# Optimization experiments

Measured on AMD Instinct MI355X. Metric: run time of the kernel, lower is better.

The kernel has to match this reference:

```python
import jax, jax.numpy as jnp
import numpy as np

N_NODES = 100000
N_EDGES = 3200000
IN_CH = 256
OUT_CH = 128


def setup_inputs() -> dict:
    key = jax.random.key(0)
    k1, k2, k3, k4, k5 = jax.random.split(key, 5)
    x = jax.random.normal(k1, (N_NODES, IN_CH), dtype=jnp.float32)
    edge_src = jax.random.randint(k2, (N_EDGES,), 0, N_NODES, dtype=jnp.int64 if jax.config.jax_enable_x64 else jnp.int32)
    edge_dst = jax.random.randint(k3, (N_EDGES,), 0, N_NODES, dtype=jnp.int64 if jax.config.jax_enable_x64 else jnp.int32)
    edge_vals = jax.random.uniform(k4, (N_EDGES,), dtype=jnp.float32)
    weight = jax.random.normal(k5, (IN_CH, OUT_CH), dtype=jnp.float32) * (2.0 / (IN_CH + OUT_CH)) ** 0.5  # glorot
    bias = jnp.zeros((OUT_CH,), dtype=jnp.float32)
    return {"x": x, "edge_src": edge_src, "edge_dst": edge_dst,
            "edge_vals": edge_vals, "weight": weight, "bias": bias}


def reference(x, edge_src, edge_dst, edge_vals, weight, bias):
    # out = A @ (x @ W) + b, with A given in COO form (edge_src=row, edge_dst=col, edge_vals)
    xw = x @ weight                                  # [N, out]
    msgs = xw[edge_dst] * edge_vals[:, None]         # gather source features, scale by edge weight
    agg = jax.ops.segment_sum(msgs, edge_src, num_segments=N_NODES)  # scatter-add to rows
    return agg + bias
```

## Files before the change

### kernel.cpp

```cpp
#include <hip/hip_runtime.h>

#define N_NODES 100000
#define N_EDGES 3200000
#define IN_CH   256
#define OUT_CH  128

#define BSH        5
#define BN         32
#define NBIN       3125
#define NBLK1      392
#define EPB1       8192
#define NS1        (NBIN * NBLK1)
#define SCAN_CHUNK 8192
#define NBLK_S1    ((NS1 + SCAN_CHUNK - 1) / SCAN_CHUNK)

#define OFF_XWB    0
#define OFF_WBF    25600000
#define OFF_CNTA   25665536
#define OFF_RPA    30565536
#define OFF_BS     35465552
#define OFF_RPN    35466576
#define OFF_PACKED 35866592

typedef __attribute__((ext_vector_type(8))) short    bf8;
typedef __attribute__((ext_vector_type(4))) float    f4;
typedef __attribute__((ext_vector_type(4))) unsigned uv4;

__device__ __forceinline__ unsigned f2bf(float f) {
    unsigned u = __float_as_uint(f);
    return (u + 0x7fffu + ((u >> 16) & 1u)) >> 16;
}

__global__ __launch_bounds__(256) void wcvt_kernel(const float* __restrict__ w,
                                                   unsigned short* __restrict__ wbf) {
    int t = threadIdx.x;
    int k = blockIdx.x * 2 + (t >> 7);
    int n = t & 127;
    wbf[n * 256 + k] = (unsigned short)f2bf(w[k * 128 + n]);
}

__global__ __launch_bounds__(256) void gemm_kernel(const float* __restrict__ x,
                                                   const unsigned short* __restrict__ wbf,
                                                   unsigned* __restrict__ xwb) {
    int wave = threadIdx.x >> 6;
    int lane = threadIdx.x & 63;
    int m = lane & 15;
    int q = lane >> 4;
    int r0 = blockIdx.x * 64 + wave * 16;

    int arow = r0 + m;
    if (arow >= N_NODES) arow = N_NODES - 1;
    const float* xr = x + (long long)arow * IN_CH + q * 8;

    f4 acc[8];
#pragma unroll
    for (int ct = 0; ct < 8; ++ct) acc[ct] = (f4){0.f, 0.f, 0.f, 0.f};

#pragma unroll
    for (int ks = 0; ks < 8; ++ks) {
        float4 xa = *(const float4*)(xr + ks * 32);
        float4 xb = *(const float4*)(xr + ks * 32 + 4);
        bf8 a;
        a[0] = (short)f2bf(xa.x); a[1] = (short)f2bf(xa.y);
        a[2] = (short)f2bf(xa.z); a[3] = (short)f2bf(xa.w);
        a[4] = (short)f2bf(xb.x); a[5] = (short)f2bf(xb.y);
        a[6] = (short)f2bf(xb.z); a[7] = (short)f2bf(xb.w);
#pragma unroll
        for (int ct = 0; ct < 8; ++ct) {
            uv4 u = *(const uv4*)&wbf[(ct * 16 + m) * 256 + ks * 32 + q * 8];
            bf8 b = __builtin_bit_cast(bf8, u);
            acc[ct] = __builtin_amdgcn_mfma_f32_16x16x32_bf16(a, b, acc[ct], 0, 0, 0);
        }
    }

#pragma unroll
    for (int ct = 0; ct < 8; ++ct) {
#pragma unroll
        for (int r = 0; r < 4; ++r) {
            float v = acc[ct][r];
            float p = __shfl_xor(v, 1, 64);
            unsigned mine = f2bf(v), oth = f2bf(p);
            if (!(m & 1)) {
                int row = r0 + q * 4 + r;
                if (row < N_NODES)
                    xwb[row * 64 + ct * 8 + (m >> 1)] = mine | (oth << 16);
            }
        }
    }
}

__global__ __launch_bounds__(1024) void h1_kernel(const int* __restrict__ src,
                                                  int* __restrict__ cntA) {
    __shared__ int lc[NBIN];
    int tid = threadIdx.x;
    for (int i = tid; i < NBIN; i += 1024) lc[i] = 0;
    __syncthreads();
#pragma unroll
    for (int k = 0; k < EPB1 / 4096; ++k) {
        int i = blockIdx.x * EPB1 + k * 4096 + tid * 4;
        if (i < N_EDGES) {
            int4 s = *(const int4*)&src[i];
            atomicAdd(&lc[s.x >> BSH], 1);
            atomicAdd(&lc[s.y >> BSH], 1);
            atomicAdd(&lc[s.z >> BSH], 1);
            atomicAdd(&lc[s.w >> BSH], 1);
        }
    }
    __syncthreads();
    for (int i = tid; i < NBIN; i += 1024)
        cntA[i * NBLK1 + blockIdx.x] = lc[i];
}

__global__ __launch_bounds__(256) void scan_s1(const int* __restrict__ cnt,
                                               int* __restrict__ bsum) {
    __shared__ int wsum[4];
    int tid = threadIdx.x, lane = tid & 63, wid = tid >> 6;
    int acc = 0;
#pragma unroll
    for (int k = 0; k < SCAN_CHUNK / 1024; ++k) {
        int i0 = blockIdx.x * SCAN_CHUNK + k * 1024 + tid * 4;
        if (i0 < NS1) {
            int4 v = *(const int4*)&cnt[i0];
            acc += v.x + v.y + v.z + v.w;
        }
    }
#pragma unroll
    for (int off = 32; off; off >>= 1) acc += __shfl_down(acc, off, 64);
    if (lane == 0) wsum[wid] = acc;
    __syncthreads();
    if (tid == 0) bsum[blockIdx.x] = wsum[0] + wsum[1] + wsum[2] + wsum[3];
}

__global__ __launch_bounds__(256) void scan_s2(int* __restrict__ bsum,
                                               int* __restrict__ rpA,
                                               int* __restrict__ rpn) {
    __shared__ int wsum[4];
    int tid = threadIdx.x, lane = tid & 63, wid = tid >> 6;
    int v = (tid < NBLK_S1) ? bsum[tid] : 0;
    int s = v;
#pragma unroll
    for (int off = 1; off < 64; off <<= 1) {
        int t = __shfl_up(s, off, 64);
        if (lane >= off) s += t;
    }
    if (lane == 63) wsum[wid] = s;
    __syncthreads();
    int w0 = wsum[0], w1 = wsum[1], w2 = wsum[2], w3 = wsum[3];
    int woff = (wid > 0 ? w0 : 0) + (wid > 1 ? w1 : 0) + (wid > 2 ? w2 : 0);
    if (tid < NBLK_S1) bsum[tid] = woff + s - v;
    if (tid == 0) {
        int tot = w0 + w1 + w2 + w3;
        rpA[NS1] = tot;
        rpn[N_NODES] = tot;
    }
}

__global__ __launch_bounds__(256) void scan_s3(const int* __restrict__ cnt,
                                               const int* __restrict__ bsum,
                                               int* __restrict__ rpA) {
    __shared__ int wsum[4];
    int tid = threadIdx.x, lane = tid & 63, wid = tid >> 6;
    int carry = bsum[blockIdx.x];
#pragma unroll
    for (int k = 0; k < SCAN_CHUNK / 1024; ++k) {
        int i0 = blockIdx.x * SCAN_CHUNK + k * 1024 + tid * 4;
        int4 v = make_int4(0, 0, 0, 0);
        if (i0 < NS1) v = *(const int4*)&cnt[i0];
        int sum4 = v.x + v.y + v.z + v.w;
        int s = sum4;
#pragma unroll
        for (int off = 1; off < 64; off <<= 1) {
            int t = __shfl_up(s, off, 64);
            if (lane >= off) s += t;
        }
        if (lane == 63) wsum[wid] = s;
        __syncthreads();
        int w0 = wsum[0], w1 = wsum[1], w2 = wsum[2], w3 = wsum[3];
        int woff = (wid > 0 ? w0 : 0) + (wid > 1 ? w1 : 0) + (wid > 2 ? w2 : 0);
        int excl = carry + woff + (s - sum4);
        if (i0 < NS1)
            *(int4*)&rpA[i0] = make_int4(excl, excl + v.x, excl + v.x + v.y,
                                         excl + v.x + v.y + v.z);
        carry += w0 + w1 + w2 + w3;
        __syncthreads();
    }
}

__global__ __launch_bounds__(1024) void b1_kernel(const int* __restrict__ src,
                                                  const int* __restrict__ dst,
                                                  const float* __restrict__ val,
                                                  const int* __restrict__ rpA,
                                                  int2* __restrict__ p1) {
    __shared__ int lcur[NBIN];
    int tid = threadIdx.x;
    for (int i = tid; i < NBIN; i += 1024)
        lcur[i] = rpA[i * NBLK1 + blockIdx.x];
    __syncthreads();
#pragma unroll
    for (int k = 0; k < EPB1 / 4096; ++k) {
        int i = blockIdx.x * EPB1 + k * 4096 + tid * 4;
        if (i < N_EDGES) {
            int4   s = *(const int4*)&src[i];
            int4   d = *(const int4*)&dst[i];
            float4 v = *(const float4*)&val[i];
            int p;
            p = atomicAdd(&lcur[s.x >> BSH], 1);
            p1[p] = make_int2(d.x | ((s.x & (BN - 1)) << 17), __float_as_int(v.x));
            p = atomicAdd(&lcur[s.y >> BSH], 1);
            p1[p] = make_int2(d.y | ((s.y & (BN - 1)) << 17), __float_as_int(v.y));
            p = atomicAdd(&lcur[s.z >> BSH], 1);
            p1[p] = make_int2(d.z | ((s.z & (BN - 1)) << 17), __float_as_int(v.z));
            p = atomicAdd(&lcur[s.w >> BSH], 1);
            p1[p] = make_int2(d.w | ((s.w & (BN - 1)) << 17), __float_as_int(v.w));
        }
    }
}

__global__ __launch_bounds__(256) void sortf_kernel(const int2* __restrict__ p1,
                                                    const int* __restrict__ rpA,
                                                    int2* __restrict__ packed,
                                                    int* __restrict__ rpn) {
    __shared__ int lcnt[BN];
    __shared__ int lcur[BN];
    int b = blockIdx.x, tid = threadIdx.x;
    int beg = rpA[b * NBLK1];
    int end = rpA[(b + 1) * NBLK1];

    if (tid < BN) lcnt[tid] = 0;
    __syncthreads();

    for (int e = beg + tid; e < end; e += 256)
        atomicAdd(&lcnt[(p1[e].x >> 17) & (BN - 1)], 1);
    __syncthreads();

    if (tid < BN) {
        int c = lcnt[tid];
        int v = c;
#pragma unroll
        for (int off = 1; off < BN; off <<= 1) {
            int t = __shfl_up(v, off, 64);
            if (tid >= off) v += t;
        }
        int excl = beg + v - c;
        lcur[tid] = excl;
        rpn[b * BN + tid] = excl;
    }
    __syncthreads();

    for (int e = beg + tid; e < end; e += 256) {
        int2 q = p1[e];
        int p = atomicAdd(&lcur[(q.x >> 17) & (BN - 1)], 1);
        packed[p] = make_int2(q.x & 0x1FFFF, q.y);
    }
}

__global__ __launch_bounds__(256) void aggregate_kernel(const int* __restrict__ rp,
                                                        const int2* __restrict__ packed,
                                                        const unsigned* __restrict__ xwb,
                                                        const float* __restrict__ bias,
                                                        float* __restrict__ out) {
    int node = blockIdx.x * 4 + (threadIdx.x >> 6);
    int lane = threadIdx.x & 63;
    float2 acc = *(const float2*)&bias[lane * 2];

    int e   = rp[node];
    int end = rp[node + 1];
    for (; e + 4 <= end; e += 4) {
        int2 p0 = packed[e + 0];
        int2 p1 = packed[e + 1];
        int2 p2 = packed[e + 2];
        int2 p3 = packed[e + 3];
        unsigned u0 = xwb[p0.x * 64 + lane];
        unsigned u1 = xwb[p1.x * 64 + lane];
        unsigned u2 = xwb[p2.x * 64 + lane];
        unsigned u3 = xwb[p3.x * 64 + lane];
        float v0 = __int_as_float(p0.y), v1 = __int_as_float(p1.y);
        float v2 = __int_as_float(p2.y), v3 = __int_as_float(p3.y);
        acc.x += v0 * __uint_as_float(u0 << 16);
        acc.y += v0 * __uint_as_float(u0 & 0xffff0000u);
        acc.x += v1 * __uint_as_float(u1 << 16);
        acc.y += v1 * __uint_as_float(u1 & 0xffff0000u);
        acc.x += v2 * __uint_as_float(u2 << 16);
        acc.y += v2 * __uint_as_float(u2 & 0xffff0000u);
        acc.x += v3 * __uint_as_float(u3 << 16);
        acc.y += v3 * __uint_as_float(u3 & 0xffff0000u);
    }
    for (; e < end; ++e) {
        int2 p = packed[e];
        unsigned u = xwb[p.x * 64 + lane];
        float v = __int_as_float(p.y);
        acc.x += v * __uint_as_float(u << 16);
        acc.y += v * __uint_as_float(u & 0xffff0000u);
    }
    *(float2*)&out[(long long)node * OUT_CH + lane * 2] = acc;
}

extern "C" void kernel_launch(void* const* d_in, const int* in_sizes, int n_in,
                              void* d_out, int out_size, void* d_ws, size_t ws_size,
                              hipStream_t stream) {
    const float* x     = (const float*)d_in[0];
    const int*   esrc  = (const int*)d_in[1];
    const int*   edst  = (const int*)d_in[2];
    const float* evals = (const float*)d_in[3];
    const float* w     = (const float*)d_in[4];
    const float* bias  = (const float*)d_in[5];
    float* out = (float*)d_out;

    char* ws = (char*)d_ws;
    unsigned*       xwb    = (unsigned*)      (ws + OFF_XWB);
    unsigned short* wbf    = (unsigned short*)(ws + OFF_WBF);
    int*            cntA   = (int*)           (ws + OFF_CNTA);
    int*            rpA    = (int*)           (ws + OFF_RPA);
    int*            bsum   = (int*)           (ws + OFF_BS);
    int*            rpn    = (int*)           (ws + OFF_RPN);
    int2*           packed = (int2*)          (ws + OFF_PACKED);
    int2*           p1     = (int2*)          d_out;

    wcvt_kernel<<<128, 256, 0, stream>>>(w, wbf);
    gemm_kernel<<<(N_NODES + 63) / 64, 256, 0, stream>>>(x, wbf, xwb);
    h1_kernel<<<NBLK1, 1024, 0, stream>>>(esrc, cntA);
    scan_s1<<<NBLK_S1, 256, 0, stream>>>(cntA, bsum);
    scan_s2<<<1, 256, 0, stream>>>(bsum, rpA, rpn);
    scan_s3<<<NBLK_S1, 256, 0, stream>>>(cntA, bsum, rpA);
    b1_kernel<<<NBLK1, 1024, 0, stream>>>(esrc, edst, evals, rpA, p1);
    sortf_kernel<<<NBIN, 256, 0, stream>>>(p1, rpA, packed, rpn);
    aggregate_kernel<<<N_NODES / 4, 256, 0, stream>>>(rpn, packed, xwb, bias, out);
}
```

Baseline: 451.8 us.

## Transpose histogram tables, cache bins in LDS, and broadcast edge records via readlane

The per-block bin counts and offsets are now written and read in block-major order, with explicit tiled transpose kernels, so the histogram and binning kernels make coalesced rather than strided global accesses. sortf stages each bin's records in shared memory when they fit, so it reads them from global once instead of twice. The aggregate kernel loads up to 64 edge records per wave with one coalesced load, then broadcasts each one with readlane and issues 8 gathers at a time. In exchange it adds two extra kernel launches and a larger workspace, and it pads the edge loop to multiples of 8; this looks safe only because out-of-range lanes hold a zero value and index 0.

```diff
diff --git a/kernel.cpp b/kernel.cpp
--- a/kernel.cpp
+++ b/kernel.cpp
@@ -13,14 +13,17 @@
 #define NS1        (NBIN * NBLK1)
 #define SCAN_CHUNK 8192
 #define NBLK_S1    ((NS1 + SCAN_CHUNK - 1) / SCAN_CHUNK)
+#define SCAP       2048
 
 #define OFF_XWB    0
 #define OFF_WBF    25600000
-#define OFF_CNTA   25665536
-#define OFF_RPA    30565536
-#define OFF_BS     35465552
-#define OFF_RPN    35466576
-#define OFF_PACKED 35866592
+#define OFF_CNTT   25665536
+#define OFF_CNTA   30565536
+#define OFF_RPA    35465536
+#define OFF_RPT    40365552
+#define OFF_BS     45265552
+#define OFF_RPN    45266576
+#define OFF_PACKED 45666592
 
 typedef __attribute__((ext_vector_type(8))) short    bf8;
 typedef __attribute__((ext_vector_type(4))) float    f4;
@@ -90,7 +93,7 @@
 }
 
 __global__ __launch_bounds__(1024) void h1_kernel(const int* __restrict__ src,
-                                                  int* __restrict__ cntA) {
+                                                  int* __restrict__ cntT) {
     __shared__ int lc[NBIN];
     int tid = threadIdx.x;
     for (int i = tid; i < NBIN; i += 1024) lc[i] = 0;
@@ -108,7 +111,26 @@
     }
     __syncthreads();
     for (int i = tid; i < NBIN; i += 1024)
-        cntA[i * NBLK1 + blockIdx.x] = lc[i];
+        cntT[blockIdx.x * NBIN + i] = lc[i];
+}
+
+__global__ __launch_bounds__(256) void transpose_kernel(const int* __restrict__ in,
+                                                        int* __restrict__ out,
+                                                        int R, int C) {
+    __shared__ int t[32][33];
+    int tx = threadIdx.x & 31, ty0 = threadIdx.x >> 5;
+    int c0 = blockIdx.x * 32, r0 = blockIdx.y * 32;
+#pragma unroll
+    for (int i = 0; i < 4; ++i) {
+        int r = r0 + ty0 + i * 8, c = c0 + tx;
+        t[ty0 + i * 8][tx] = (r < R && c < C) ? in[r * C + c] : 0;
+    }
+    __syncthreads();
+#pragma unroll
+    for (int i = 0; i < 4; ++i) {
+        int c = c0 + ty0 + i * 8, r = r0 + tx;
+        if (c < C && r < R) out[c * R + r] = t[tx][ty0 + i * 8];
+    }
 }
 
 __global__ __launch_bounds__(256) void scan_s1(const int* __restrict__ cnt,
@@ -189,12 +211,12 @@
 __global__ __launch_bounds__(1024) void b1_kernel(const int* __restrict__ src,
                                                   const int* __restrict__ dst,
                                                   const float* __restrict__ val,
-                                                  const int* __restrict__ rpA,
+                                                  const int* __restrict__ rpT,
                                                   int2* __restrict__ p1) {
     __shared__ int lcur[NBIN];
     int tid = threadIdx.x;
     for (int i = tid; i < NBIN; i += 1024)
-        lcur[i] = rpA[i * NBLK1 + blockIdx.x];
+        lcur[i] = rpT[blockIdx.x * NBIN + i];
     __syncthreads();
 #pragma unroll
     for (int k = 0; k < EPB1 / 4096; ++k) {
@@ -220,17 +242,27 @@
                                                     const int* __restrict__ rpA,
                                                     int2* __restrict__ packed,
                                                     int* __restrict__ rpn) {
-    __shared__ int lcnt[BN];
-    __shared__ int lcur[BN];
+    __shared__ int  lcnt[BN];
+    __shared__ int  lcur[BN];
+    __shared__ int2 sbuf[SCAP];
     int b = blockIdx.x, tid = threadIdx.x;
     int beg = rpA[b * NBLK1];
     int end = rpA[(b + 1) * NBLK1];
+    int n = end - beg;
 
     if (tid < BN) lcnt[tid] = 0;
     __syncthreads();
 
-    for (int e = beg + tid; e < end; e += 256)
-        atomicAdd(&lcnt[(p1[e].x >> 17) & (BN - 1)], 1);
+    if (n <= SCAP) {
+        for (int e = tid; e < n; e += 256) {
+            int2 q = p1[beg + e];
+            sbuf[e] = q;
+            atomicAdd(&lcnt[(q.x >> 17) & (BN - 1)], 1);
+        }
+    } else {
+        for (int e = beg + tid; e < end; e += 256)
+            atomicAdd(&lcnt[(p1[e].x >> 17) & (BN - 1)], 1);
+    }
     __syncthreads();
 
     if (tid < BN) {
@@ -247,10 +279,18 @@
     }
     __syncthreads();
 
-    for (int e = beg + tid; e < end; e += 256) {
-        int2 q = p1[e];
-        int p = atomicAdd(&lcur[(q.x >> 17) & (BN - 1)], 1);
-        packed[p] = make_int2(q.x & 0x1FFFF, q.y);
+    if (n <= SCAP) {
+        for (int e = tid; e < n; e += 256) {
+            int2 q = sbuf[e];
+            int p = atomicAdd(&lcur[(q.x >> 17) & (BN - 1)], 1);
+            packed[p] = make_int2(q.x & 0x1FFFF, q.y);
+        }
+    } else {
+        for (int e = beg + tid; e < end; e += 256) {
+            int2 q = p1[e];
+            int p = atomicAdd(&lcur[(q.x >> 17) & (BN - 1)], 1);
+            packed[p] = make_int2(q.x & 0x1FFFF, q.y);
+        }
     }
 }
 
@@ -263,34 +303,28 @@
     int lane = threadIdx.x & 63;
     float2 acc = *(const float2*)&bias[lane * 2];
 
-    int e   = rp[node];
+    int beg = rp[node];
     int end = rp[node + 1];
-    for (; e + 4 <= end; e += 4) {
-        int2 p0 = packed[e + 0];
-        int2 p1 = packed[e + 1];
-        int2 p2 = packed[e + 2];
-        int2 p3 = packed[e + 3];
-        unsigned u0 = xwb[p0.x * 64 + lane];
-        unsigned u1 = xwb[p1.x * 64 + lane];
-        unsigned u2 = xwb[p2.x * 64 + lane];
-        unsigned u3 = xwb[p3.x * 64 + lane];
-        float v0 = __int_as_float(p0.y), v1 = __int_as_float(p1.y);
-        float v2 = __int_as_float(p2.y), v3 = __int_as_float(p3.y);
-        acc.x += v0 * __uint_as_float(u0 << 16);
-        acc.y += v0 * __uint_as_float(u0 & 0xffff0000u);
-        acc.x += v1 * __uint_as_float(u1 << 16);
-        acc.y += v1 * __uint_as_float(u1 & 0xffff0000u);
-        acc.x += v2 * __uint_as_float(u2 << 16);
-        acc.y += v2 * __uint_as_float(u2 & 0xffff0000u);
-        acc.x += v3 * __uint_as_float(u3 << 16);
-        acc.y += v3 * __uint_as_float(u3 & 0xffff0000u);
-    }
-    for (; e < end; ++e) {
-        int2 p = packed[e];
-        unsigned u = xwb[p.x * 64 + lane];
-        float v = __int_as_float(p.y);
-        acc.x += v * __uint_as_float(u << 16);
-        acc.y += v * __uint_as_float(u & 0xffff0000u);
+    for (int t = beg; t < end; t += 64) {
+        int2 rec = make_int2(0, 0);
+        if (t + lane < end) rec = packed[t + lane];
+        int cnt = end - t; if (cnt > 64) cnt = 64;
+        int cnt8 = (cnt + 7) & ~7;
+        for (int j = 0; j < cnt8; j += 8) {
+            unsigned u[8]; float vv[8];
+#pragma unroll
+            for (int k = 0; k < 8; ++k) {
+                int d  = __builtin_amdgcn_readlane(rec.x, j + k);
+                int vb = __builtin_amdgcn_readlane(rec.y, j + k);
+                vv[k] = __int_as_float(vb);
+                u[k]  = xwb[d * 64 + lane];
+            }
+#pragma unroll
+            for (int k = 0; k < 8; ++k) {
+                acc.x += vv[k] * __uint_as_float(u[k] << 16);
+                acc.y += vv[k] * __uint_as_float(u[k] & 0xffff0000u);
+            }
+        }
     }
     *(float2*)&out[(long long)node * OUT_CH + lane * 2] = acc;
 }
@@ -309,8 +343,10 @@
     char* ws = (char*)d_ws;
     unsigned*       xwb    = (unsigned*)      (ws + OFF_XWB);
     unsigned short* wbf    = (unsigned short*)(ws + OFF_WBF);
+    int*            cntT   = (int*)           (ws + OFF_CNTT);
     int*            cntA   = (int*)           (ws + OFF_CNTA);
     int*            rpA    = (int*)           (ws + OFF_RPA);
+    int*            rpT    = (int*)           (ws + OFF_RPT);
     int*            bsum   = (int*)           (ws + OFF_BS);
     int*            rpn    = (int*)           (ws + OFF_RPN);
     int2*           packed = (int2*)          (ws + OFF_PACKED);
@@ -318,11 +354,15 @@
 
     wcvt_kernel<<<128, 256, 0, stream>>>(w, wbf);
     gemm_kernel<<<(N_NODES + 63) / 64, 256, 0, stream>>>(x, wbf, xwb);
-    h1_kernel<<<NBLK1, 1024, 0, stream>>>(esrc, cntA);
+    h1_kernel<<<NBLK1, 1024, 0, stream>>>(esrc, cntT);
+    transpose_kernel<<<dim3((NBIN + 31) / 32, (NBLK1 + 31) / 32), 256, 0, stream>>>(
+        cntT, cntA, NBLK1, NBIN);
     scan_s1<<<NBLK_S1, 256, 0, stream>>>(cntA, bsum);
     scan_s2<<<1, 256, 0, stream>>>(bsum, rpA, rpn);
     scan_s3<<<NBLK_S1, 256, 0, stream>>>(cntA, bsum, rpA);
-    b1_kernel<<<NBLK1, 1024, 0, stream>>>(esrc, edst, evals, rpA, p1);
+    transpose_kernel<<<dim3((NBLK1 + 31) / 32, (NBIN + 31) / 32), 256, 0, stream>>>(
+        rpA, rpT, NBIN, NBLK1);
+    b1_kernel<<<NBLK1, 1024, 0, stream>>>(esrc, edst, evals, rpT, p1);
     sortf_kernel<<<NBIN, 256, 0, stream>>>(p1, rpA, packed, rpn);
     aggregate_kernel<<<N_NODES / 4, 256, 0, stream>>>(rpn, packed, xwb, bias, out);
 }
```

Result: faster. 430.0 us (-4.8%).
